# Kernel tuning notes

Hardware: AMD Instinct MI355X
Metric: run time of the kernel (lower is better)

## Reference

```python
import jax, jax.numpy as jnp
import numpy as np

B, L, E, H = 8192, 64, 128, 8  # batch, max seq len, info_size, head_num
HD = E // H                    # head dim


def setup_inputs() -> dict:
    key = jax.random.key(0)
    k1, k2, k3, k4, k5, k6 = jax.random.split(key, 6)
    inter_info = jax.random.normal(k1, (B, L, E), dtype=jnp.float32)
    # ragged lengths in [1, L] (each sample has at least the query vector)
    lengths = jax.random.randint(k2, (B,), 1, L + 1, dtype=jnp.int32)
    s = 1.0 / np.sqrt(E)
    in_proj_w = jax.random.uniform(k3, (3 * E, E), dtype=jnp.float32, minval=-s, maxval=s)
    in_proj_b = jnp.zeros((3 * E,), dtype=jnp.float32)
    out_proj_w = jax.random.uniform(k4, (E, E), dtype=jnp.float32, minval=-s, maxval=s)
    out_proj_b = jnp.zeros((E,), dtype=jnp.float32)
    return {"inter_info": inter_info, "lengths": lengths,
            "in_proj_w": in_proj_w, "in_proj_b": in_proj_b,
            "out_proj_w": out_proj_w, "out_proj_b": out_proj_b}


def reference(inter_info, lengths, in_proj_w, in_proj_b, out_proj_w, out_proj_b):
    # Per sample: query = first vector, keys/values = all (valid) vectors.
    # Equivalent to torch nn.MultiheadAttention with 1 query per sample.
    Wq, Wk, Wv = in_proj_w[:E], in_proj_w[E:2 * E], in_proj_w[2 * E:]
    bq, bk, bv = in_proj_b[:E], in_proj_b[E:2 * E], in_proj_b[2 * E:]

    query_info = inter_info[:, 0]                                  # [B, E]
    q = (query_info @ Wq.T + bq).reshape(B, H, HD)                 # [B, H, hd]
    k = (inter_info @ Wk.T + bk).reshape(B, L, H, HD)              # [B, L, H, hd]
    v = (inter_info @ Wv.T + bv).reshape(B, L, H, HD)

    scores = jnp.einsum('bhd,blhd->bhl', q, k) / np.sqrt(HD)       # [B, H, L]
    valid = jnp.arange(L)[None, :] < lengths[:, None]              # [B, L]
    scores = jnp.where(valid[:, None, :], scores, -jnp.inf)
    attn = jax.nn.softmax(scores, axis=-1)                         # [B, H, L]

    ctx = jnp.einsum('bhl,blhd->bhd', attn, v).reshape(B, E)       # [B, E]
    attn_hidden = ctx @ out_proj_w.T + out_proj_b                  # [B, E]
    return attn_hidden, query_info
```

## Files before the change

### kernel.cpp

```cpp
#include <hip/hip_runtime.h>
#include <hip/hip_bf16.h>


typedef unsigned int  u32;
typedef unsigned short u16;
typedef unsigned long long u64;

#define XR  136
#define XR4 17
#define YR  136
#define UR  136
#define SCR 68
#define QR  132
#define YSR 1032

#define WS_U_OFF 0u
#define WS_C_OFF 16777216u
#define WS_Y_OFF 17825792u
#define WS_NEED  34603008u

typedef __attribute__((ext_vector_type(8))) __bf16 bf16x8;
typedef __attribute__((ext_vector_type(4))) float  f32x4;

__device__ __forceinline__ float blo(u32 u) { return __uint_as_float(u << 16); }
__device__ __forceinline__ float bhi(u32 u) { return __uint_as_float(u & 0xffff0000u); }
__device__ __forceinline__ float b2f(u16 u) { return __uint_as_float(((u32)u) << 16); }
__device__ __forceinline__ u16 f2b(float f) {
  union { __hip_bfloat16 h; u16 u; } cv; cv.h = __float2bfloat16(f); return cv.u;
}
__device__ __forceinline__ u32 pack2(float a, float b) {
  return (u32)f2b(a) | ((u32)f2b(b) << 16);
}

template<bool BF>
__device__ __forceinline__ uint4 wfrag(const void* p, size_t off) {
  if (BF) {
    return *(const uint4*)((const u16*)p + off);
  } else {
    const float4* q4 = (const float4*)((const float*)p + off);
    float4 a = q4[0], b = q4[1];
    uint4 v;
    v.x = pack2(a.x, a.y); v.y = pack2(a.z, a.w);
    v.z = pack2(b.x, b.y); v.w = pack2(b.z, b.w);
    return v;
  }
}
template<bool BF>
__device__ __forceinline__ void load4(const void* p, size_t off, float* o) {
  if (BF) {
    uint2 v = *(const uint2*)((const u16*)p + off);
    o[0]=blo(v.x); o[1]=bhi(v.x); o[2]=blo(v.y); o[3]=bhi(v.y);
  } else {
    float4 v = *(const float4*)((const float*)p + off);
    o[0]=v.x; o[1]=v.y; o[2]=v.z; o[3]=v.w;
  }
}
template<bool BF>
__device__ __forceinline__ float lds1(const void* p, size_t off) {
  return BF ? b2f(((const u16*)p)[off]) : ((const float*)p)[off];
}

struct __align__(16) SmemK1 {
  u16   X0s[8 * XR];
  float q[8 * QR];
  int   isbf;
};

template<bool BF>
__device__ __forceinline__ void k1_body(SmemK1& S, int b0, int t,
    const void* inter, const void* w_in, const void* b_in,
    u16* Uws, float* Cws)
{
  const int lane = t & 63, w = t >> 6;

  if (t < 128) {
    const int i = t >> 4, ci = t & 15;
    const size_t bidx = (size_t)(b0 + i);
    uint4 v;
    if (BF) {
      v = ((const uint4*)inter)[bidx * 1024 + ci];
    } else {
      const float4* src = (const float4*)inter + bidx * 2048 + ci * 2;
      float4 a = src[0], b = src[1];
      v.x = pack2(a.x, a.y); v.y = pack2(a.z, a.w);
      v.z = pack2(b.x, b.y); v.w = pack2(b.z, b.w);
    }
    *(uint4*)&S.X0s[i * XR + ci * 8] = v;
  }
  __syncthreads();

  {
    const int r15 = lane & 15, e = w * 16 + r15;
    const int kb = (lane >> 4) * 8, rbase = (lane >> 4) * 4;
    f32x4 acc = {0.f, 0.f, 0.f, 0.f};
#pragma unroll
    for (int kc = 0; kc < 4; ++kc) {
      union { uint4 u4; bf16x8 b8; } A, Bf;
      A.u4  = *(const uint4*)&S.X0s[(r15 & 7) * XR + kc * 32 + kb];
      Bf.u4 = wfrag<BF>(w_in, (size_t)e * 128 + kc * 32 + kb);
      acc = __builtin_amdgcn_mfma_f32_16x16x32_bf16(A.b8, Bf.b8, acc, 0, 0, 0);
    }
    const float bq  = lds1<BF>(b_in, e);
    const float bkv = lds1<BF>(b_in, 128 + e);
    float cs[4];
#pragma unroll
    for (int r = 0; r < 4; ++r) {
      float qv = acc[r] + bq;
      if (rbase < 8) S.q[(rbase + r) * QR + e] = qv;
      cs[r] = qv * bkv;
    }
#pragma unroll
    for (int off = 1; off < 16; off <<= 1) {
      cs[0] += __shfl_xor(cs[0], off, 64);
      cs[1] += __shfl_xor(cs[1], off, 64);
      cs[2] += __shfl_xor(cs[2], off, 64);
      cs[3] += __shfl_xor(cs[3], off, 64);
    }
    if (r15 == 0 && rbase < 8) {
#pragma unroll
      for (int r = 0; r < 4; ++r)
        Cws[(size_t)(b0 + rbase + r) * 8 + w] = cs[r];
    }
  }
  __syncthreads();

  {
    const int hh = t >> 8, bt = (t >> 5) & 7, cc = t & 31;
#pragma unroll
    for (int hi = 0; hi < 4; ++hi) {
      const int h = hh * 4 + hi;
      float a0 = 0.f, a1 = 0.f, a2 = 0.f, a3 = 0.f;
#pragma unroll
      for (int d = 0; d < 16; ++d) {
        float w4[4]; load4<BF>(w_in, (size_t)(128 + h * 16 + d) * 128 + cc * 4, w4);
        float q0 = S.q[bt * QR + h * 16 + d];
        a0 = fmaf(w4[0], q0, a0); a1 = fmaf(w4[1], q0, a1);
        a2 = fmaf(w4[2], q0, a2); a3 = fmaf(w4[3], q0, a3);
      }
      *(uint2*)&Uws[(size_t)(b0 + bt) * 1024 + h * 128 + cc * 4] =
          make_uint2(pack2(a0, a1), pack2(a2, a3));
    }
  }
}

__global__ __launch_bounds__(512, 4) void k1_kernel(
    const void* inter, const void* w_in, const void* b_in,
    u16* Uws, float* Cws)
{
  __shared__ SmemK1 S;
  const int t = threadIdx.x;
  const int b0 = blockIdx.x * 8;
  if (t < 64) {
    float v = b2f(((const u16*)inter)[t]);
    bool bad = !(fabsf(v) < 1000.f);
    u64 m = __ballot(bad);
    if (t == 0) S.isbf = (m == 0ull) ? 1 : 0;
  }
  __syncthreads();
  if (S.isbf) k1_body<true >(S, b0, t, inter, w_in, b_in, Uws, Cws);
  else        k1_body<false>(S, b0, t, inter, w_in, b_in, Uws, Cws);
}

struct __align__(16) SmemK2 {
  u16   Xs[2][64 * XR];
  u16   u[2][8 * UR];
  u16   y[2][8 * YR];
  float sc[2][8][SCR];
  float c[2][8];
  int   isbf;
};

template<bool BF>
__device__ __forceinline__ void k2_body(SmemK2& S, int b0, int t,
    const void* inter, const int* lengths, const u16* Uws, const float* Cws,
    u16* Yws, void* out)
{
  const int len0 = lengths[b0];
  const int len1 = lengths[b0 + 1];
  const int lane = t & 63, w = t >> 6;

#pragma unroll
  for (int r = 0; r < 4; ++r) {
    int g = t + 512 * r;
    int tile = g >> 10, gg = g & 1023, l = gg >> 4, ci = gg & 15;
    uint4 v = make_uint4(0u, 0u, 0u, 0u);
    if (l < (tile ? len1 : len0)) {
      if (BF) {
        v = ((const uint4*)inter)[(size_t)b0 * 1024 + g];
      } else {
        const float4* src = (const float4*)inter + (size_t)b0 * 2048;
        float4 a = src[g * 2], bb = src[g * 2 + 1];
        v.x = pack2(a.x, a.y); v.y = pack2(a.z, a.w);
        v.z = pack2(bb.x, bb.y); v.w = pack2(bb.z, bb.w);
      }
    }
    ((uint4*)S.Xs[tile])[l * XR4 + ci] = v;
  }
  if (t < 256) {
    const int bt = t >> 7, rem = t & 127, h = rem >> 4, ci = rem & 15;
    uint4 v = ((const uint4*)Uws)[(size_t)(b0 + bt) * 128 + h * 16 + ci];
    *(uint4*)&S.u[bt][h * UR + ci * 8] = v;
  } else if (t < 272) {
    const int i = t - 256, bt = i >> 3, h = i & 7;
    S.c[bt][h] = Cws[(size_t)(b0 + bt) * 8 + h];
  }
  __syncthreads();

  {
    const int bt = w >> 2, mt = w & 3;
    const int arow = mt * 16 + (lane & 15);
    const int col  = lane & 15;
    const int kb   = (lane >> 4) * 8;
    const bool hv  = (col < 8);
    f32x4 acc = {0.f, 0.f, 0.f, 0.f};
#pragma unroll
    for (int kc = 0; kc < 4; ++kc) {
      union { uint4 u4; bf16x8 b8; } a, bu;
      a.u4  = *(const uint4*)&S.Xs[bt][arow * XR + kc * 32 + kb];
      bu.u4 = *(const uint4*)&S.u[bt][(col & 7) * UR + kc * 32 + kb];
      if (!hv) bu.u4 = make_uint4(0u, 0u, 0u, 0u);
      acc = __builtin_amdgcn_mfma_f32_16x16x32_bf16(a.b8, bu.b8, acc, 0, 0, 0);
    }
    if (hv) {
      const int l0 = mt * 16 + (lane >> 4) * 4;
      const float cadd = S.c[bt][col];
      f32x4 o;
      o[0] = (acc[0] + cadd) * 0.25f;
      o[1] = (acc[1] + cadd) * 0.25f;
      o[2] = (acc[2] + cadd) * 0.25f;
      o[3] = (acc[3] + cadd) * 0.25f;
      *(f32x4*)&S.sc[bt][col][l0] = o;
    }
  }
  __syncthreads();

  {
    const int bt = t >> 8, h = (t >> 5) & 7, sub = t & 31;
    const int len = bt ? len1 : len0;
    const int l0 = sub, l1 = sub + 32;
    float s0 = S.sc[bt][h][l0], s1 = S.sc[bt][h][l1];
    const bool v0 = l0 < len, v1 = l1 < len;
    float m = fmaxf(v0 ? s0 : -INFINITY, v1 ? s1 : -INFINITY);
#pragma unroll
    for (int off = 16; off > 0; off >>= 1) m = fmaxf(m, __shfl_xor(m, off, 32));
    float e0 = v0 ? __expf(s0 - m) : 0.f;
    float e1 = v1 ? __expf(s1 - m) : 0.f;
    float s = e0 + e1;
#pragma unroll
    for (int off = 16; off > 0; off >>= 1) s += __shfl_xor(s, off, 32);
    float inv = 1.f / s;
    S.sc[bt][h][l0] = e0 * inv;
    S.sc[bt][h][l1] = e1 * inv;
  }
  __syncthreads();

  {
    const int bt = w >> 2, j0 = (w & 3) * 32;
    const int hA = (lane & 15) < 8 ? (lane & 15) : 7;
    const int l8 = (lane >> 4) * 8;
    const int jc0 = j0 + (lane & 15), jc1 = jc0 + 16;
    const int len = bt ? len1 : len0;
    f32x4 acc0 = {0.f,0.f,0.f,0.f}, acc1 = {0.f,0.f,0.f,0.f};
    const u16* xb = S.Xs[bt];
    {
      const int lb = l8;
      float4 pa = *(const float4*)&S.sc[bt][hA][lb];
      float4 pb = *(const float4*)&S.sc[bt][hA][lb + 4];
      union { u32 u[4]; bf16x8 b; } A, B0, B1;
      A.u[0] = pack2(pa.x, pa.y); A.u[1] = pack2(pa.z, pa.w);
      A.u[2] = pack2(pb.x, pb.y); A.u[3] = pack2(pb.z, pb.w);
#pragma unroll
      for (int jj = 0; jj < 4; ++jj) {
        u32 lo0 = xb[(lb+2*jj)*XR + jc0], hi0 = xb[(lb+2*jj+1)*XR + jc0];
        u32 lo1 = xb[(lb+2*jj)*XR + jc1], hi1 = xb[(lb+2*jj+1)*XR + jc1];
        B0.u[jj] = lo0 | (hi0 << 16);
        B1.u[jj] = lo1 | (hi1 << 16);
      }
      acc0 = __builtin_amdgcn_mfma_f32_16x16x32_bf16(A.b, B0.b, acc0, 0, 0, 0);
      acc1 = __builtin_amdgcn_mfma_f32_16x16x32_bf16(A.b, B1.b, acc1, 0, 0, 0);
    }
    if (len > 32) {
      const int lb = 32 + l8;
      float4 pa = *(const float4*)&S.sc[bt][hA][lb];
      float4 pb = *(const float4*)&S.sc[bt][hA][lb + 4];
      union { u32 u[4]; bf16x8 b; } A, B0, B1;
      A.u[0] = pack2(pa.x, pa.y); A.u[1] = pack2(pa.z, pa.w);
      A.u[2] = pack2(pb.x, pb.y); A.u[3] = pack2(pb.z, pb.w);
#pragma unroll
      for (int jj = 0; jj < 4; ++jj) {
        u32 lo0 = xb[(lb+2*jj)*XR + jc0], hi0 = xb[(lb+2*jj+1)*XR + jc0];
        u32 lo1 = xb[(lb+2*jj)*XR + jc1], hi1 = xb[(lb+2*jj+1)*XR + jc1];
        B0.u[jj] = lo0 | (hi0 << 16);
        B1.u[jj] = lo1 | (hi1 << 16);
      }
      acc0 = __builtin_amdgcn_mfma_f32_16x16x32_bf16(A.b, B0.b, acc0, 0, 0, 0);
      acc1 = __builtin_amdgcn_mfma_f32_16x16x32_bf16(A.b, B1.b, acc1, 0, 0, 0);
    }
    const int rbase = (lane >> 4) * 4;
    if (rbase < 8) {
#pragma unroll
      for (int r = 0; r < 4; ++r) {
        S.y[bt][(rbase + r) * YR + j0 + (lane & 15)]      = f2b(acc0[r]);
        S.y[bt][(rbase + r) * YR + j0 + 16 + (lane & 15)] = f2b(acc1[r]);
      }
    }
  }
  __syncthreads();

  if (t < 256) {
    const int bt = t >> 7, rem = t & 127, h = rem >> 4, ci = rem & 15;
    uint4 v = *(const uint4*)&S.y[bt][h * YR + ci * 8];
    ((uint4*)Yws)[(size_t)(b0 + bt) * 128 + h * 16 + ci] = v;
  } else {
    const int i = t - 256, bt = i >> 7, e = i & 127;
    size_t o1 = (size_t)8192 * 128 + (size_t)(b0 + bt) * 128 + e;
    u16 xv = S.Xs[bt][e];
    if (BF) ((u16*)out)[o1] = xv;
    else    ((float*)out)[o1] = b2f(xv);
  }
}

__global__ __launch_bounds__(512, 4) void k2_kernel(
    const void* inter, const int* __restrict__ lengths,
    const u16* Uws, const float* Cws, u16* Yws, void* out)
{
  __shared__ SmemK2 S;
  const int t = threadIdx.x;
  const int b0 = blockIdx.x * 2;
  if (t < 64) {
    float v = b2f(((const u16*)inter)[t]);
    bool bad = !(fabsf(v) < 1000.f);
    u64 m = __ballot(bad);
    if (t == 0) S.isbf = (m == 0ull) ? 1 : 0;
  }
  __syncthreads();
  if (S.isbf) k2_body<true >(S, b0, t, inter, lengths, Uws, Cws, Yws, out);
  else        k2_body<false>(S, b0, t, inter, lengths, Uws, Cws, Yws, out);
}

struct __align__(16) SmemK3 {
  u16 ys[16 * YSR];
  u16 ctx[16 * 136];
  int isbf;
};

template<bool BF>
__device__ __forceinline__ void k3_body(SmemK3& S, int b0, int t,
    const u16* Yws, const void* w_in, const void* b_in,
    const void* w_out, const void* b_out, void* out)
{
  const int lane = t & 63, w = t >> 6;

#pragma unroll
  for (int r = 0; r < 4; ++r) {
    int idx = t + 512 * r;
    int row = idx >> 7, ci = idx & 127;
    uint4 v = ((const uint4*)Yws)[(size_t)(b0 + row) * 128 + ci];
    *(uint4*)&S.ys[row * YSR + ci * 8] = v;
  }
  __syncthreads();

  {
    const int col = lane & 15, kb = (lane >> 4) * 8, rbase = (lane >> 4) * 4;
    f32x4 acc = {0.f, 0.f, 0.f, 0.f};
#pragma unroll
    for (int kc = 0; kc < 4; ++kc) {
      union { uint4 u4; bf16x8 b8; } A, Bf;
      A.u4  = *(const uint4*)&S.ys[col * YSR + w * 128 + kc * 32 + kb];
      Bf.u4 = wfrag<BF>(w_in, (size_t)(256 + w * 16 + col) * 128 + kc * 32 + kb);
      acc = __builtin_amdgcn_mfma_f32_16x16x32_bf16(A.b8, Bf.b8, acc, 0, 0, 0);
    }
    const float bv = lds1<BF>(b_in, 256 + w * 16 + col);
#pragma unroll
    for (int r = 0; r < 4; ++r)
      S.ctx[(rbase + r) * 136 + w * 16 + col] = f2b(acc[r] + bv);
  }
  __syncthreads();

  {
    const int col = lane & 15, kb = (lane >> 4) * 8, rbase = (lane >> 4) * 4;
    f32x4 acc = {0.f, 0.f, 0.f, 0.f};
#pragma unroll
    for (int kc = 0; kc < 4; ++kc) {
      union { uint4 u4; bf16x8 b8; } A, Bf;
      A.u4  = *(const uint4*)&S.ctx[col * 136 + kc * 32 + kb];
      Bf.u4 = wfrag<BF>(w_out, (size_t)(w * 16 + col) * 128 + kc * 32 + kb);
      acc = __builtin_amdgcn_mfma_f32_16x16x32_bf16(A.b8, Bf.b8, acc, 0, 0, 0);
    }
    const float bo = lds1<BF>(b_out, w * 16 + col);
#pragma unroll
    for (int r = 0; r < 4; ++r) {
      float v = acc[r] + bo;
      size_t oo = (size_t)(b0 + rbase + r) * 128 + w * 16 + col;
      if (BF) ((u16*)out)[oo] = f2b(v);
      else    ((float*)out)[oo] = v;
    }
  }
}

__global__ __launch_bounds__(512, 4) void k3_kernel(
    const u16* Yws, const void* w_in, const void* b_in,
    const void* w_out, const void* b_out, void* out)
{
  __shared__ SmemK3 S;
  const int t = threadIdx.x;
  const int b0 = blockIdx.x * 16;
  if (t < 64) {
    float v = b2f(((const u16*)w_out)[t]);
    bool bad = !(fabsf(v) < 1000.f);
    u64 m = __ballot(bad);
    if (t == 0) S.isbf = (m == 0ull) ? 1 : 0;
  }
  __syncthreads();
  if (S.isbf) k3_body<true >(S, b0, t, Yws, w_in, b_in, w_out, b_out, out);
  else        k3_body<false>(S, b0, t, Yws, w_in, b_in, w_out, b_out, out);
}

struct __align__(16) SmemM {
  u16   Xs[2][64 * XR];
  u16   u[2][8 * UR];
  u16   y[2][8 * YR];
  float q[2][128];
  float sc[2][8][SCR];
  float c[2][8];
  float ctx[2][128];
  int   isbf;
};

template<bool BF>
__device__ __forceinline__ void mono_body(SmemM& S, int b0, int t,
    const void* inter, const int* lengths, const void* w_in, const void* b_in,
    const void* w_out, const void* b_out, void* out)
{
  const int len0 = lengths[b0];
  const int len1 = lengths[b0 + 1];
  const int lane = t & 63, w = t >> 6;

#pragma unroll
  for (int r = 0; r < 4; ++r) {
    int g = t + 512 * r;
    int tile = g >> 10, gg = g & 1023, l = gg >> 4, ci = gg & 15;
    uint4 v = make_uint4(0u, 0u, 0u, 0u);
    if (l < (tile ? len1 : len0)) {
      if (BF) {
        v = ((const uint4*)inter)[(size_t)b0 * 1024 + g];
      } else {
        const float4* src = (const float4*)inter + (size_t)b0 * 2048;
        float4 a = src[g * 2], b = src[g * 2 + 1];
        v.x = pack2(a.x, a.y); v.y = pack2(a.z, a.w);
        v.z = pack2(b.x, b.y); v.w = pack2(b.z, b.w);
      }
    }
    ((uint4*)S.Xs[tile])[l * XR4 + ci] = v;
  }
  __syncthreads();

  {
    const int e = w * 16 + (lane & 15);
    const int btc = (lane & 15) < 2 ? (lane & 15) : 1;
    const int kb = (lane >> 4) * 8;
    f32x4 acc = {0.f, 0.f, 0.f, 0.f};
#pragma unroll
    for (int kc = 0; kc < 4; ++kc) {
      union { uint4 u4; bf16x8 b8; } A, Bf;
      A.u4  = *(const uint4*)&S.Xs[btc][kc * 32 + kb];
      Bf.u4 = wfrag<BF>(w_in, (size_t)e * 128 + kc * 32 + kb);
      acc = __builtin_amdgcn_mfma_f32_16x16x32_bf16(A.b8, Bf.b8, acc, 0, 0, 0);
    }
    if (lane < 16) {
      float bq = lds1<BF>(b_in, e);
      S.q[0][e] = acc[0] + bq;
      S.q[1][e] = acc[1] + bq;
    }
  }
  __syncthreads();

  {
    const int bt = t >> 8, h = (t >> 5) & 7, cc = t & 31;
    float a0=0.f,a1=0.f,a2=0.f,a3=0.f;
#pragma unroll
    for (int d = 0; d < 16; ++d) {
      float w4[4]; load4<BF>(w_in, (size_t)(128 + h * 16 + d) * 128 + cc * 4, w4);
      float q0 = S.q[bt][h * 16 + d];
      a0 = fmaf(w4[0], q0, a0); a1 = fmaf(w4[1], q0, a1);
      a2 = fmaf(w4[2], q0, a2); a3 = fmaf(w4[3], q0, a3);
    }
    *(uint2*)&S.u[bt][h * UR + cc * 4] = make_uint2(pack2(a0, a1), pack2(a2, a3));
    if (cc == 0) {
      float c0 = 0.f;
      for (int d = 0; d < 16; ++d)
        c0 += S.q[bt][h * 16 + d] * lds1<BF>(b_in, 128 + h * 16 + d);
      S.c[bt][h] = c0;
    }
  }
  __syncthreads();

  {
    const int bt = w >> 2, mt = w & 3;
    const int arow = mt * 16 + (lane & 15);
    const int col  = lane & 15;
    const int kb   = (lane >> 4) * 8;
    const bool hv  = (col < 8);
    f32x4 acc = {0.f, 0.f, 0.f, 0.f};
#pragma unroll
    for (int kc = 0; kc < 4; ++kc) {
      union { uint4 u4; bf16x8 b8; } a, bu;
      a.u4  = *(const uint4*)&S.Xs[bt][arow * XR + kc * 32 + kb];
      bu.u4 = *(const uint4*)&S.u[bt][(col & 7) * UR + kc * 32 + kb];
      if (!hv) bu.u4 = make_uint4(0u, 0u, 0u, 0u);
      acc = __builtin_amdgcn_mfma_f32_16x16x32_bf16(a.b8, bu.b8, acc, 0, 0, 0);
    }
    if (hv) {
      const int l0 = mt * 16 + (lane >> 4) * 4;
      const float cadd = S.c[bt][col];
      f32x4 o;
      o[0] = (acc[0] + cadd) * 0.25f;
      o[1] = (acc[1] + cadd) * 0.25f;
      o[2] = (acc[2] + cadd) * 0.25f;
      o[3] = (acc[3] + cadd) * 0.25f;
      *(f32x4*)&S.sc[bt][col][l0] = o;
    }
  }
  __syncthreads();

  {
    const int bt = t >> 8, h = (t >> 5) & 7, sub = t & 31;
    const int len = bt ? len1 : len0;
    const int l0 = sub, l1 = sub + 32;
    float s0 = S.sc[bt][h][l0], s1 = S.sc[bt][h][l1];
    const bool v0 = l0 < len, v1 = l1 < len;
    float m = fmaxf(v0 ? s0 : -INFINITY, v1 ? s1 : -INFINITY);
#pragma unroll
    for (int off = 16; off > 0; off >>= 1) m = fmaxf(m, __shfl_xor(m, off, 32));
    float e0 = v0 ? __expf(s0 - m) : 0.f;
    float e1 = v1 ? __expf(s1 - m) : 0.f;
    float s = e0 + e1;
#pragma unroll
    for (int off = 16; off > 0; off >>= 1) s += __shfl_xor(s, off, 32);
    float inv = 1.f / s;
    S.sc[bt][h][l0] = e0 * inv;
    S.sc[bt][h][l1] = e1 * inv;
  }
  __syncthreads();

  {
    const int bt = w >> 2, j0 = (w & 3) * 32;
    const int hA = (lane & 15) < 8 ? (lane & 15) : 7;
    const int l8 = (lane >> 4) * 8;
    const int jc0 = j0 + (lane & 15), jc1 = jc0 + 16;
    const int len = bt ? len1 : len0;
    f32x4 acc0 = {0.f,0.f,0.f,0.f}, acc1 = {0.f,0.f,0.f,0.f};
    const u16* xb = S.Xs[bt];
    {
      const int lb = l8;
      float4 pa = *(const float4*)&S.sc[bt][hA][lb];
      float4 pb = *(const float4*)&S.sc[bt][hA][lb + 4];
      union { u32 u[4]; bf16x8 b; } A, B0, B1;
      A.u[0] = pack2(pa.x, pa.y); A.u[1] = pack2(pa.z, pa.w);
      A.u[2] = pack2(pb.x, pb.y); A.u[3] = pack2(pb.z, pb.w);
#pragma unroll
      for (int jj = 0; jj < 4; ++jj) {
        u32 lo0 = xb[(lb+2*jj)*XR + jc0], hi0 = xb[(lb+2*jj+1)*XR + jc0];
        u32 lo1 = xb[(lb+2*jj)*XR + jc1], hi1 = xb[(lb+2*jj+1)*XR + jc1];
        B0.u[jj] = lo0 | (hi0 << 16);
        B1.u[jj] = lo1 | (hi1 << 16);
      }
      acc0 = __builtin_amdgcn_mfma_f32_16x16x32_bf16(A.b, B0.b, acc0, 0, 0, 0);
      acc1 = __builtin_amdgcn_mfma_f32_16x16x32_bf16(A.b, B1.b, acc1, 0, 0, 0);
    }
    if (len > 32) {
      const int lb = 32 + l8;
      float4 pa = *(const float4*)&S.sc[bt][hA][lb];
      float4 pb = *(const float4*)&S.sc[bt][hA][lb + 4];
      union { u32 u[4]; bf16x8 b; } A, B0, B1;
      A.u[0] = pack2(pa.x, pa.y); A.u[1] = pack2(pa.z, pa.w);
      A.u[2] = pack2(pb.x, pb.y); A.u[3] = pack2(pb.z, pb.w);
#pragma unroll
      for (int jj = 0; jj < 4; ++jj) {
        u32 lo0 = xb[(lb+2*jj)*XR + jc0], hi0 = xb[(lb+2*jj+1)*XR + jc0];
        u32 lo1 = xb[(lb+2*jj)*XR + jc1], hi1 = xb[(lb+2*jj+1)*XR + jc1];
        B0.u[jj] = lo0 | (hi0 << 16);
        B1.u[jj] = lo1 | (hi1 << 16);
      }
      acc0 = __builtin_amdgcn_mfma_f32_16x16x32_bf16(A.b, B0.b, acc0, 0, 0, 0);
      acc1 = __builtin_amdgcn_mfma_f32_16x16x32_bf16(A.b, B1.b, acc1, 0, 0, 0);
    }
    const int rbase = (lane >> 4) * 4;
    if (rbase < 8) {
#pragma unroll
      for (int r = 0; r < 4; ++r) {
        S.y[bt][(rbase + r) * YR + j0 + (lane & 15)]      = f2b(acc0[r]);
        S.y[bt][(rbase + r) * YR + j0 + 16 + (lane & 15)] = f2b(acc1[r]);
      }
    }
  }
  __syncthreads();

  {
    const int e = w * 16 + (lane & 15);
    const int btc = (lane & 15) < 2 ? (lane & 15) : 1;
    const int kb = (lane >> 4) * 8;
    f32x4 acc = {0.f, 0.f, 0.f, 0.f};
#pragma unroll
    for (int kc = 0; kc < 4; ++kc) {
      union { uint4 u4; bf16x8 b8; } A, Bf;
      A.u4  = *(const uint4*)&S.y[btc][w * YR + kc * 32 + kb];
      Bf.u4 = wfrag<BF>(w_in, (size_t)(256 + e) * 128 + kc * 32 + kb);
      acc = __builtin_amdgcn_mfma_f32_16x16x32_bf16(A.b8, Bf.b8, acc, 0, 0, 0);
    }
    if (lane < 16) {
      S.ctx[0][e] = acc[0] + lds1<BF>(b_in, 256 + e);
      S.ctx[1][e] = acc[1] + lds1<BF>(b_in, 256 + e);
    }
  }
  __syncthreads();

  {
    const int e = w * 16 + (lane & 15);
    const int btc = (lane & 15) < 2 ? (lane & 15) : 1;
    const int kb = (lane >> 4) * 8;
    f32x4 acc = {0.f, 0.f, 0.f, 0.f};
#pragma unroll
    for (int kc = 0; kc < 4; ++kc) {
      union { u32 u[4]; bf16x8 b; } A;
      union { uint4 u4; bf16x8 b8; } Bf;
      float4 ca = *(const float4*)&S.ctx[btc][kc * 32 + kb];
      float4 cb = *(const float4*)&S.ctx[btc][kc * 32 + kb + 4];
      A.u[0] = pack2(ca.x, ca.y); A.u[1] = pack2(ca.z, ca.w);
      A.u[2] = pack2(cb.x, cb.y); A.u[3] = pack2(cb.z, cb.w);
      Bf.u4 = wfrag<BF>(w_out, (size_t)e * 128 + kc * 32 + kb);
      acc = __builtin_amdgcn_mfma_f32_16x16x32_bf16(A.b, Bf.b8, acc, 0, 0, 0);
    }
    if (lane < 16) {
      float bo = lds1<BF>(b_out, e);
      float a0 = acc[0] + bo, a1 = acc[1] + bo;
      if (BF) {
        ((u16*)out)[(size_t)b0 * 128 + e]       = f2b(a0);
        ((u16*)out)[(size_t)(b0 + 1) * 128 + e] = f2b(a1);
      } else {
        ((float*)out)[(size_t)b0 * 128 + e]       = a0;
        ((float*)out)[(size_t)(b0 + 1) * 128 + e] = a1;
      }
    } else if (lane < 48) {
      const int bt = (lane >> 4) - 1;
      size_t o1 = (size_t)8192 * 128 + (size_t)(b0 + bt) * 128 + e;
      u16 xv = S.Xs[bt][e];
      if (BF) ((u16*)out)[o1] = xv;
      else    ((float*)out)[o1] = b2f(xv);
    }
  }
}

__global__ __launch_bounds__(512, 4) void mono_kernel(
    const void* inter, const int* __restrict__ lengths,
    const void* w_in, const void* b_in, const void* w_out, const void* b_out,
    void* out)
{
  __shared__ SmemM S;
  const int t = threadIdx.x;
  const int b0 = blockIdx.x * 2;
  if (t < 64) {
    float v = b2f(((const u16*)inter)[t]);
    bool bad = !(fabsf(v) < 1000.f);
    u64 m = __ballot(bad);
    if (t == 0) S.isbf = (m == 0ull) ? 1 : 0;
  }
  __syncthreads();
  if (S.isbf) mono_body<true >(S, b0, t, inter, lengths, w_in, b_in, w_out, b_out, out);
  else        mono_body<false>(S, b0, t, inter, lengths, w_in, b_in, w_out, b_out, out);
}

extern "C" void kernel_launch(void* const* d_in, const int* in_sizes, int n_in,
                              void* d_out, int out_size, void* d_ws, size_t ws_size,
                              hipStream_t stream) {
  if (d_ws && ws_size >= (size_t)WS_NEED) {
    u16*   Uws = (u16*)((char*)d_ws + WS_U_OFF);
    float* Cws = (float*)((char*)d_ws + WS_C_OFF);
    u16*   Yws = (u16*)((char*)d_ws + WS_Y_OFF);
    k1_kernel<<<dim3(1024), dim3(512), 0, stream>>>(
        d_in[0], d_in[2], d_in[3], Uws, Cws);
    k2_kernel<<<dim3(4096), dim3(512), 0, stream>>>(
        d_in[0], (const int*)d_in[1], Uws, Cws, Yws, d_out);
    k3_kernel<<<dim3(512), dim3(512), 0, stream>>>(
        Yws, d_in[2], d_in[3], d_in[4], d_in[5], d_out);
  } else {
    mono_kernel<<<dim3(4096), dim3(512), 0, stream>>>(
        d_in[0], (const int*)d_in[1], d_in[2], d_in[3], d_in[4], d_in[5], d_out);
  }
}
```

Measured before the change: 380.8 us.

## Skip padded score tiles, write Y and query rows directly, reuse weights across batches

In k1, the U projection now gives each thread four batch rows per weight load, so each weight vector fetched from global memory is reused across samples. In k2, the score MFMA is skipped for 16-row tiles that lie wholly beyond the sample length. The Y tile is written straight to global memory instead of being staged through shared memory, which removes a barrier and an LDS buffer. The query-row output is copied exactly from the source during the load phase, removing the bf16 round trip in the fp32 path, and the direct Y stores are narrower and less coalesced.

```diff
diff --git a/kernel.cpp b/kernel.cpp
--- a/kernel.cpp
+++ b/kernel.cpp
@@ -125,20 +125,27 @@
   __syncthreads();
 
   {
-    const int hh = t >> 8, bt = (t >> 5) & 7, cc = t & 31;
-#pragma unroll
-    for (int hi = 0; hi < 4; ++hi) {
-      const int h = hh * 4 + hi;
-      float a0 = 0.f, a1 = 0.f, a2 = 0.f, a3 = 0.f;
-#pragma unroll
-      for (int d = 0; d < 16; ++d) {
-        float w4[4]; load4<BF>(w_in, (size_t)(128 + h * 16 + d) * 128 + cc * 4, w4);
-        float q0 = S.q[bt * QR + h * 16 + d];
-        a0 = fmaf(w4[0], q0, a0); a1 = fmaf(w4[1], q0, a1);
-        a2 = fmaf(w4[2], q0, a2); a3 = fmaf(w4[3], q0, a3);
-      }
+    const int h = t >> 6, rem = t & 63;
+    const int cc = rem >> 1, s = rem & 1;
+    float a[4][4] = {{0.f,0.f,0.f,0.f},{0.f,0.f,0.f,0.f},
+                     {0.f,0.f,0.f,0.f},{0.f,0.f,0.f,0.f}};
+#pragma unroll
+    for (int d = 0; d < 16; ++d) {
+      float w4[4]; load4<BF>(w_in, (size_t)(128 + h * 16 + d) * 128 + cc * 4, w4);
+#pragma unroll
+      for (int bi = 0; bi < 4; ++bi) {
+        float q0 = S.q[(s * 4 + bi) * QR + h * 16 + d];
+        a[bi][0] = fmaf(w4[0], q0, a[bi][0]);
+        a[bi][1] = fmaf(w4[1], q0, a[bi][1]);
+        a[bi][2] = fmaf(w4[2], q0, a[bi][2]);
+        a[bi][3] = fmaf(w4[3], q0, a[bi][3]);
+      }
+    }
+#pragma unroll
+    for (int bi = 0; bi < 4; ++bi) {
+      const int bt = s * 4 + bi;
       *(uint2*)&Uws[(size_t)(b0 + bt) * 1024 + h * 128 + cc * 4] =
-          make_uint2(pack2(a0, a1), pack2(a2, a3));
+          make_uint2(pack2(a[bi][0], a[bi][1]), pack2(a[bi][2], a[bi][3]));
     }
   }
 }
@@ -164,7 +171,6 @@
 struct __align__(16) SmemK2 {
   u16   Xs[2][64 * XR];
   u16   u[2][8 * UR];
-  u16   y[2][8 * YR];
   float sc[2][8][SCR];
   float c[2][8];
   int   isbf;
@@ -187,9 +193,15 @@
     if (l < (tile ? len1 : len0)) {
       if (BF) {
         v = ((const uint4*)inter)[(size_t)b0 * 1024 + g];
+        if (l == 0)
+          ((uint4*)out)[131072 + (size_t)(b0 + tile) * 16 + ci] = v;
       } else {
         const float4* src = (const float4*)inter + (size_t)b0 * 2048;
         float4 a = src[g * 2], bb = src[g * 2 + 1];
+        if (l == 0) {
+          float4* o4 = (float4*)out + 262144 + (size_t)(b0 + tile) * 32 + ci * 2;
+          o4[0] = a; o4[1] = bb;
+        }
         v.x = pack2(a.x, a.y); v.y = pack2(a.z, a.w);
         v.z = pack2(bb.x, bb.y); v.w = pack2(bb.z, bb.w);
       }
@@ -208,28 +220,31 @@
 
   {
     const int bt = w >> 2, mt = w & 3;
-    const int arow = mt * 16 + (lane & 15);
-    const int col  = lane & 15;
-    const int kb   = (lane >> 4) * 8;
-    const bool hv  = (col < 8);
-    f32x4 acc = {0.f, 0.f, 0.f, 0.f};
-#pragma unroll
-    for (int kc = 0; kc < 4; ++kc) {
-      union { uint4 u4; bf16x8 b8; } a, bu;
-      a.u4  = *(const uint4*)&S.Xs[bt][arow * XR + kc * 32 + kb];
-      bu.u4 = *(const uint4*)&S.u[bt][(col & 7) * UR + kc * 32 + kb];
-      if (!hv) bu.u4 = make_uint4(0u, 0u, 0u, 0u);
-      acc = __builtin_amdgcn_mfma_f32_16x16x32_bf16(a.b8, bu.b8, acc, 0, 0, 0);
-    }
-    if (hv) {
-      const int l0 = mt * 16 + (lane >> 4) * 4;
-      const float cadd = S.c[bt][col];
-      f32x4 o;
-      o[0] = (acc[0] + cadd) * 0.25f;
-      o[1] = (acc[1] + cadd) * 0.25f;
-      o[2] = (acc[2] + cadd) * 0.25f;
-      o[3] = (acc[3] + cadd) * 0.25f;
-      *(f32x4*)&S.sc[bt][col][l0] = o;
+    const int len = bt ? len1 : len0;
+    if (mt * 16 < len) {
+      const int arow = mt * 16 + (lane & 15);
+      const int col  = lane & 15;
+      const int kb   = (lane >> 4) * 8;
+      const bool hv  = (col < 8);
+      f32x4 acc = {0.f, 0.f, 0.f, 0.f};
+#pragma unroll
+      for (int kc = 0; kc < 4; ++kc) {
+        union { uint4 u4; bf16x8 b8; } a, bu;
+        a.u4  = *(const uint4*)&S.Xs[bt][arow * XR + kc * 32 + kb];
+        bu.u4 = *(const uint4*)&S.u[bt][(col & 7) * UR + kc * 32 + kb];
+        if (!hv) bu.u4 = make_uint4(0u, 0u, 0u, 0u);
+        acc = __builtin_amdgcn_mfma_f32_16x16x32_bf16(a.b8, bu.b8, acc, 0, 0, 0);
+      }
+      if (hv) {
+        const int l0 = mt * 16 + (lane >> 4) * 4;
+        const float cadd = S.c[bt][col];
+        f32x4 o;
+        o[0] = (acc[0] + cadd) * 0.25f;
+        o[1] = (acc[1] + cadd) * 0.25f;
+        o[2] = (acc[2] + cadd) * 0.25f;
+        o[3] = (acc[3] + cadd) * 0.25f;
+        *(f32x4*)&S.sc[bt][col][l0] = o;
+      }
     }
   }
   __syncthreads();
@@ -298,25 +313,13 @@
     }
     const int rbase = (lane >> 4) * 4;
     if (rbase < 8) {
+      u16* yo = Yws + (size_t)(b0 + bt) * 1024;
 #pragma unroll
       for (int r = 0; r < 4; ++r) {
-        S.y[bt][(rbase + r) * YR + j0 + (lane & 15)]      = f2b(acc0[r]);
-        S.y[bt][(rbase + r) * YR + j0 + 16 + (lane & 15)] = f2b(acc1[r]);
-      }
-    }
-  }
-  __syncthreads();
-
-  if (t < 256) {
-    const int bt = t >> 7, rem = t & 127, h = rem >> 4, ci = rem & 15;
-    uint4 v = *(const uint4*)&S.y[bt][h * YR + ci * 8];
-    ((uint4*)Yws)[(size_t)(b0 + bt) * 128 + h * 16 + ci] = v;
-  } else {
-    const int i = t - 256, bt = i >> 7, e = i & 127;
-    size_t o1 = (size_t)8192 * 128 + (size_t)(b0 + bt) * 128 + e;
-    u16 xv = S.Xs[bt][e];
-    if (BF) ((u16*)out)[o1] = xv;
-    else    ((float*)out)[o1] = b2f(xv);
+        yo[(rbase + r) * 128 + j0 + (lane & 15)]      = f2b(acc0[r]);
+        yo[(rbase + r) * 128 + j0 + 16 + (lane & 15)] = f2b(acc1[r]);
+      }
+    }
   }
 }
 
```

Result: faster. 372.2 us (-2.3%).
